# Optimization experiments

Measured on AMD Instinct MI355X. Metric: run time of the kernel, lower is better.

## Reference

```python
import jax, jax.numpy as jnp
import numpy as np

N, L, H, D_HEAD, P = 2, 1024, 8, 64, 1
DIM = H * D_HEAD


def setup_inputs() -> dict:
    key0 = jax.random.key(0)
    ks = jax.random.split(key0, 7)
    query = jax.random.normal(ks[0], (N, L, DIM), dtype=jnp.float32)
    key = jax.random.normal(ks[1], (N, L, DIM), dtype=jnp.float32)
    scale = 1.0 / np.sqrt(DIM)
    Wq = jax.random.normal(ks[2], (DIM, DIM), dtype=jnp.float32) * scale
    Wk = jax.random.normal(ks[3], (DIM, DIM), dtype=jnp.float32) * scale
    Wv = jax.random.normal(ks[4], (DIM, DIM), dtype=jnp.float32) * scale
    position_weight = jax.random.uniform(ks[5], (H, P, D_HEAD), dtype=jnp.float32) * 2 - 1
    position_bias = jax.random.uniform(ks[6], (H, D_HEAD), dtype=jnp.float32) * 2 - 1
    return {"query": query, "key": key, "Wq": Wq, "Wk": Wk, "Wv": Wv,
            "position_weight": position_weight, "position_bias": position_bias}


def _kernel_fn(x):
    # _log_exp_kernel: positive feature map log(1 + exp(x)) (softplus)
    return jax.nn.softplus(x)


def _causal_term(qf, kf, v):
    """Linear-complexity causal attention term.
    qf, kf: (N,H,L,d) feature-mapped query/key; v: (N,H,L,d) values.
    Returns numerator (N,H,L,d) and denominator (N,H,L)."""
    # cumulative key-value outer products: (N,H,L,d,d)
    kv = jnp.cumsum(jnp.einsum('nhkd,nhke->nhkde', kf, v), axis=2)
    num = jnp.einsum('nhqd,nhqde->nhqe', qf, kv)
    den = jnp.einsum('nhqd,nhqd->nhq', qf, jnp.cumsum(kf, axis=2))
    return num, den


def reference(query, key, Wq, Wk, Wv, position_weight, position_bias):
    n, lq, dim = query.shape
    lk = key.shape[1]
    h, p, d = position_weight.shape
    kernel = _kernel_fn
    # projections (torch Linear: x @ W.T), reshape to heads, transpose to (N,H,L,d)
    q = kernel((query @ Wq.T).reshape(n, lq, h, d)).transpose(0, 2, 1, 3)
    k = kernel((key @ Wk.T).reshape(n, lk, h, d)).transpose(0, 2, 1, 3)
    v = ((key @ Wv.T).reshape(n, lk, h, d)).transpose(0, 2, 1, 3)
    # default positions: arange, expanded to (N,L,P)
    qpos = jnp.broadcast_to(jnp.arange(lq, dtype=query.dtype)[None, :, None], (n, lq, p))
    kpos = jnp.broadcast_to(jnp.arange(lk, dtype=key.dtype)[None, :, None], (n, lk, p))
    pq = jnp.einsum('nlp,hpd->nhld', qpos, position_weight) \
         + jax.nn.sigmoid(position_bias)[None, :, None, :] * jnp.pi
    pk = jnp.einsum('nlp,hpd->nhld', kpos, position_weight)
    # three branches: cos, sin, plain (trig identity split of cos(pq - pk) RPE)
    num_c, den_c = _causal_term(q * jnp.cos(pq), k * jnp.cos(pk), v)
    num_s, den_s = _causal_term(q * jnp.sin(pq), k * jnp.sin(pk), v)
    num_p, den_p = _causal_term(q, k, v)
    num = num_c + num_s + num_p
    den = den_c + den_s + den_p
    attention = num / den[..., None]  # scaled=True
    return attention.transpose(0, 2, 1, 3).reshape(n, lq, dim)
```

## Files before the change

### kernel.cpp

```cpp
#include <hip/hip_runtime.h>

#define LSEQ   1024
#define NHEAD  8
#define DH     64
#define DIM    512
#define DF     192
#define LDB    72
#define LDQ    200
#define LDV    72

typedef __attribute__((ext_vector_type(8))) short short8;
typedef __attribute__((ext_vector_type(4))) float floatx4;

__device__ __forceinline__ unsigned short bf16_rne(float x) {
    unsigned int u = __float_as_uint(x);
    u += 0x7FFFu + ((u >> 16) & 1u);
    return (unsigned short)(u >> 16);
}
__device__ __forceinline__ unsigned int pk_bf16(float lo, float hi) {
    unsigned int d;
    asm("v_cvt_pk_bf16_f32 %0, %1, %2" : "=v"(d) : "v"(lo), "v"(hi));
    return d;
}
__device__ __forceinline__ float softplus_fast(float x) {
    return (x > 15.f) ? x : __logf(1.f + __expf(x));
}

__global__ __launch_bounds__(256) void proj_kernel(
    const float* __restrict__ query, const float* __restrict__ key,
    const float* __restrict__ Wq, const float* __restrict__ Wk,
    const float* __restrict__ Wv,
    const float* __restrict__ pw, const float* __restrict__ pb,
    unsigned short* __restrict__ qf, unsigned short* __restrict__ kf,
    unsigned short* __restrict__ vbuf)
{
    const int mt  = blockIdx.x;
    const int ot  = blockIdx.y;
    const int sel = blockIdx.z;
    const int t   = threadIdx.x;

    const float* __restrict__ X = (sel == 0) ? query : key;
    const float* __restrict__ W = (sel == 0) ? Wq : (sel == 1) ? Wk : Wv;

    __shared__ unsigned short As[64 * LDB];
    __shared__ unsigned short Bs[64 * LDB];

    const int m0 = mt * 64, o0 = ot * 64;
    const int lane = t & 63, wave = t >> 6;
    const int quad = lane >> 4, l16 = lane & 15;
    const int wm = wave >> 1, wn = wave & 1;

    const int srow = t >> 2;
    const int sc16 = (t & 3) * 16;

    floatx4 acc[2][2];
    #pragma unroll
    for (int i = 0; i < 2; ++i)
        #pragma unroll
        for (int j = 0; j < 2; ++j) acc[i][j] = (floatx4){0.f, 0.f, 0.f, 0.f};

    float4 ax[4], bx4[4];
    #pragma unroll
    for (int i = 0; i < 4; ++i) {
        ax[i]  = *(const float4*)&X[(size_t)(m0 + srow) * DIM + sc16 + i * 4];
        bx4[i] = *(const float4*)&W[(size_t)(o0 + srow) * DIM + sc16 + i * 4];
    }

    for (int kt = 0; kt < DIM; kt += 64) {
        __syncthreads();
        {
            unsigned int ua[8], ub[8];
            #pragma unroll
            for (int i = 0; i < 4; ++i) {
                ua[2*i]   = pk_bf16(ax[i].x, ax[i].y);
                ua[2*i+1] = pk_bf16(ax[i].z, ax[i].w);
                ub[2*i]   = pk_bf16(bx4[i].x, bx4[i].y);
                ub[2*i+1] = pk_bf16(bx4[i].z, bx4[i].w);
            }
            *(uint4*)&As[srow * LDB + sc16]     = *(uint4*)&ua[0];
            *(uint4*)&As[srow * LDB + sc16 + 8] = *(uint4*)&ua[4];
            *(uint4*)&Bs[srow * LDB + sc16]     = *(uint4*)&ub[0];
            *(uint4*)&Bs[srow * LDB + sc16 + 8] = *(uint4*)&ub[4];
        }
        __syncthreads();

        if (kt + 64 < DIM) {
            #pragma unroll
            for (int i = 0; i < 4; ++i) {
                ax[i]  = *(const float4*)&X[(size_t)(m0 + srow) * DIM + kt + 64 + sc16 + i * 4];
                bx4[i] = *(const float4*)&W[(size_t)(o0 + srow) * DIM + kt + 64 + sc16 + i * 4];
            }
        }

        #pragma unroll
        for (int s = 0; s < 2; ++s) {
            short8 af[2], bf[2];
            #pragma unroll
            for (int mi = 0; mi < 2; ++mi)
                af[mi] = *(const short8*)&As[(wm * 32 + mi * 16 + l16) * LDB + s * 32 + quad * 8];
            #pragma unroll
            for (int ni = 0; ni < 2; ++ni)
                bf[ni] = *(const short8*)&Bs[(wn * 32 + ni * 16 + l16) * LDB + s * 32 + quad * 8];
            #pragma unroll
            for (int ni = 0; ni < 2; ++ni)
                #pragma unroll
                for (int mi = 0; mi < 2; ++mi)
                    acc[mi][ni] = __builtin_amdgcn_mfma_f32_16x16x32_bf16(af[mi], bf[ni], acc[mi][ni], 0, 0, 0);
        }
    }

    const int h = ot;
    const float PI_ = 3.14159265358979323846f;
    const int n_ = m0 >> 10;

    if (sel == 2) {
        __syncthreads();
        #pragma unroll
        for (int mi = 0; mi < 2; ++mi)
            #pragma unroll
            for (int ni = 0; ni < 2; ++ni) {
                const int d = wn * 32 + ni * 16 + l16;
                #pragma unroll
                for (int r = 0; r < 4; ++r) {
                    const int ml = wm * 32 + mi * 16 + quad * 4 + r;
                    As[ml * LDB + d] = bf16_rne(acc[mi][ni][r]);
                }
            }
        __syncthreads();
        const int d = t >> 2, mq = (t & 3) * 16;
        const int l0 = m0 & (LSEQ - 1);
        unsigned short col[16];
        #pragma unroll
        for (int j = 0; j < 16; ++j) col[j] = As[(mq + j) * LDB + d];
        unsigned short* dst = &vbuf[((size_t)(n_ * NHEAD + h) * DH + d) * LSEQ + l0 + mq];
        *(short8*)&dst[0] = *(short8*)&col[0];
        *(short8*)&dst[8] = *(short8*)&col[8];
    } else {
        unsigned short* __restrict__ obuf = (sel == 0) ? qf : kf;
        #pragma unroll
        for (int ni = 0; ni < 2; ++ni) {
            const int d = wn * 32 + ni * 16 + l16;
            const float w = pw[h * DH + d];
            const float bias = (sel == 0) ? PI_ / (1.f + __expf(-pb[h * DH + d])) : 0.f;
            float s1, c1; sincosf(w, &s1, &c1);
            const float c2  = c1*c1 - s1*s1,  s2  = 2.f*c1*s1;
            const float c4  = c2*c2 - s2*s2,  s4  = 2.f*c2*s2;
            const float c8  = c4*c4 - s4*s4,  s8  = 2.f*c4*s4;
            const float c16 = c8*c8 - s8*s8,  s16 = 2.f*c8*s8;
            const int lb = (m0 & (LSEQ - 1)) + wm * 32 + quad * 4;
            float sb, cb; sincosf((float)lb * w + bias, &sb, &cb);
            #pragma unroll
            for (int mi = 0; mi < 2; ++mi) {
                float cc = cb, ss = sb;
                #pragma unroll
                for (int r = 0; r < 4; ++r) {
                    const int l = lb + mi * 16 + r;
                    const float val = softplus_fast(acc[mi][ni][r]);
                    const size_t ob = ((size_t)(n_ * NHEAD + h) * LSEQ + l) * DF + d;
                    obuf[ob]          = bf16_rne(val);
                    obuf[ob + DH]     = bf16_rne(val * cc);
                    obuf[ob + 2*DH]   = bf16_rne(val * ss);
                    const float nc = cc * c1 - ss * s1;
                    ss = ss * c1 + cc * s1; cc = nc;
                }
                const float nb = cb * c16 - sb * s16;
                sb = sb * c16 + cb * s16; cb = nb;
            }
        }
    }
}

__global__ __launch_bounds__(256) void attn_kernel(
    const unsigned short* __restrict__ qf, const unsigned short* __restrict__ kf,
    const unsigned short* __restrict__ vbuf,
    float* __restrict__ outp)
{
    const int b  = blockIdx.x;
    const int nh = (b & 7) * 2 + ((b >> 3) & 1);
    const int p  = (b >> 4) & 15;
    const int z  = b >> 8;
    const int lt = z ? (31 - p) : p;
    const int n  = nh >> 3;
    const int h  = nh & (NHEAD - 1);
    const int t  = threadIdx.x;
    const int lane = t & 63, wave = t >> 6;
    const int quad = lane >> 4, l16 = lane & 15;
    const int wm = wave >> 1, wn = wave & 1;

    __shared__ unsigned short kL[64 * LDQ];
    __shared__ unsigned short vT[64 * LDV];
    __shared__ unsigned short scA[32 * LDV];
    __shared__ float denL[2][32];
    __shared__ float inv32[32];

    const size_t fbase = (size_t)nh * LSEQ;
    const int nkt = (lt >> 1) + 1;
    const int diag_kt = lt >> 1;

    short8 qreg[6];
    {
        const unsigned short* qrow = &qf[(fbase + lt * 32 + wm * 16 + l16) * DF + quad * 8];
        #pragma unroll
        for (int kk = 0; kk < 6; ++kk)
            qreg[kk] = *(const short8*)&qrow[kk * 32];
    }

    int kr[6], kc[6];
    #pragma unroll
    for (int c = 0; c < 6; ++c) {
        const int idx = c * 256 + t;
        kr[c] = idx / 24;
        kc[c] = (idx % 24) * 8;
    }
    const unsigned short* kfb = &kf[fbase * DF];
    const int ve = t >> 2, vk = (t & 3) * 16;
    const unsigned short* vfb = &vbuf[((size_t)nh * DH + ve) * LSEQ + vk];

    short8 kpre[6], vpre[2];
    #pragma unroll
    for (int c = 0; c < 6; ++c)
        kpre[c] = *(const short8*)&kfb[(size_t)kr[c] * DF + kc[c]];
    vpre[0] = *(const short8*)&vfb[0];
    vpre[1] = *(const short8*)&vfb[8];
    #pragma unroll
    for (int c = 0; c < 6; ++c)
        *(short8*)&kL[kr[c] * LDQ + kc[c]] = kpre[c];
    *(short8*)&vT[ve * LDV + vk]     = vpre[0];
    *(short8*)&vT[ve * LDV + vk + 8] = vpre[1];
    __syncthreads();

    floatx4 accN[2];
    accN[0] = (floatx4){0.f, 0.f, 0.f, 0.f};
    accN[1] = (floatx4){0.f, 0.f, 0.f, 0.f};
    float den4[4] = {0.f, 0.f, 0.f, 0.f};

    for (int kt = 0; kt < nkt; ++kt) {
        const bool pf = (kt + 1 < nkt);
        if (pf) {
            const size_t koff = (size_t)(kt + 1) * 64 * DF;
            #pragma unroll
            for (int c = 0; c < 6; ++c)
                kpre[c] = *(const short8*)&kfb[koff + (size_t)kr[c] * DF + kc[c]];
            vpre[0] = *(const short8*)&vfb[(kt + 1) * 64];
            vpre[1] = *(const short8*)&vfb[(kt + 1) * 64 + 8];
        }

        floatx4 accS[2];
        accS[0] = (floatx4){0.f, 0.f, 0.f, 0.f};
        accS[1] = (floatx4){0.f, 0.f, 0.f, 0.f};
        #pragma unroll
        for (int kk = 0; kk < 6; ++kk) {
            #pragma unroll
            for (int ni = 0; ni < 2; ++ni) {
                const short8 bfr = *(const short8*)&kL[(wn * 32 + ni * 16 + l16) * LDQ + kk * 32 + quad * 8];
                accS[ni] = __builtin_amdgcn_mfma_f32_16x16x32_bf16(qreg[kk], bfr, accS[ni], 0, 0, 0);
            }
        }

        const bool diag = (kt == diag_kt);
        #pragma unroll
        for (int ni = 0; ni < 2; ++ni) {
            const int kcolL = wn * 32 + ni * 16 + l16;
            const int kcolG = kt * 64 + kcolL;
            #pragma unroll
            for (int r = 0; r < 4; ++r) {
                const int lrowL = wm * 16 + quad * 4 + r;
                float sval = accS[ni][r];
                if (diag && kcolG > lt * 32 + lrowL) sval = 0.f;
                den4[r] += sval;
                scA[lrowL * LDV + kcolL] = bf16_rne(sval);
            }
        }
        __syncthreads();

        #pragma unroll
        for (int kk = 0; kk < 2; ++kk) {
            const short8 a = *(const short8*)&scA[(wm * 16 + l16) * LDV + kk * 32 + quad * 8];
            #pragma unroll
            for (int ni = 0; ni < 2; ++ni) {
                const short8 bfr = *(const short8*)&vT[(wn * 32 + ni * 16 + l16) * LDV + kk * 32 + quad * 8];
                accN[ni] = __builtin_amdgcn_mfma_f32_16x16x32_bf16(a, bfr, accN[ni], 0, 0, 0);
            }
        }
        __syncthreads();

        if (pf) {
            #pragma unroll
            for (int c = 0; c < 6; ++c)
                *(short8*)&kL[kr[c] * LDQ + kc[c]] = kpre[c];
            *(short8*)&vT[ve * LDV + vk]     = vpre[0];
            *(short8*)&vT[ve * LDV + vk + 8] = vpre[1];
            __syncthreads();
        }
    }

    #pragma unroll
    for (int r = 0; r < 4; ++r) {
        float s = den4[r];
        s += __shfl_xor(s, 1);
        s += __shfl_xor(s, 2);
        s += __shfl_xor(s, 4);
        s += __shfl_xor(s, 8);
        if (l16 == 0) denL[wn][wm * 16 + quad * 4 + r] = s;
    }
    __syncthreads();
    if (t < 32) inv32[t] = 1.f / (denL[0][t] + denL[1][t]);
    __syncthreads();

    #pragma unroll
    for (int ni = 0; ni < 2; ++ni) {
        const int e = wn * 32 + ni * 16 + l16;
        #pragma unroll
        for (int r = 0; r < 4; ++r) {
            const int row = wm * 16 + quad * 4 + r;
            outp[((size_t)n * LSEQ + lt * 32 + row) * DIM + h * DH + e] =
                accN[ni][r] * inv32[row];
        }
    }
}

extern "C" void kernel_launch(void* const* d_in, const int* in_sizes, int n_in,
                              void* d_out, int out_size, void* d_ws, size_t ws_size,
                              hipStream_t stream) {
    const float* query = (const float*)d_in[0];
    const float* key   = (const float*)d_in[1];
    const float* Wq    = (const float*)d_in[2];
    const float* Wk    = (const float*)d_in[3];
    const float* Wv    = (const float*)d_in[4];
    const float* pw    = (const float*)d_in[5];
    const float* pb    = (const float*)d_in[6];

    unsigned short* U = (unsigned short*)d_ws;
    unsigned short* qf   = U;
    unsigned short* kf   = U + 3145728;
    unsigned short* vbuf = U + 6291456;

    proj_kernel<<<dim3(32, 8, 3), 256, 0, stream>>>(
        query, key, Wq, Wk, Wv, pw, pb, qf, kf, vbuf);
    attn_kernel<<<dim3(512, 1, 1), 256, 0, stream>>>(
        qf, kf, vbuf, (float*)d_out);
}
```

Baseline: 105.4 us.

## Halve query tile to 16 rows and double attention grid

The attention kernel now gives each block a 16-row query tile instead of 32 and launches 1024 blocks instead of 512. Each wave handles one 16-column slice of the key tile rather than a 2x2 wave grid, and the launch bounds ask for 4 blocks per CU. MFMA sections are wrapped in s_setprio to favour matrix issue. This raises parallelism and occupancy on the causal triangular workload, but every K/V tile is now loaded from global memory twice as often in total, and the work per barrier is smaller.

```diff
diff --git a/kernel.cpp b/kernel.cpp
--- a/kernel.cpp
+++ b/kernel.cpp
@@ -170,36 +170,35 @@
     }
 }
 
-__global__ __launch_bounds__(256) void attn_kernel(
+__global__ __launch_bounds__(256, 4) void attn_kernel(
     const unsigned short* __restrict__ qf, const unsigned short* __restrict__ kf,
     const unsigned short* __restrict__ vbuf,
     float* __restrict__ outp)
 {
     const int b  = blockIdx.x;
     const int nh = (b & 7) * 2 + ((b >> 3) & 1);
-    const int p  = (b >> 4) & 15;
-    const int z  = b >> 8;
-    const int lt = z ? (31 - p) : p;
+    const int p  = (b >> 4) & 31;
+    const int z  = b >> 9;
+    const int lt = z ? (63 - p) : p;
     const int n  = nh >> 3;
     const int h  = nh & (NHEAD - 1);
     const int t  = threadIdx.x;
-    const int lane = t & 63, wave = t >> 6;
+    const int lane = t & 63, w = t >> 6;
     const int quad = lane >> 4, l16 = lane & 15;
-    const int wm = wave >> 1, wn = wave & 1;
 
     __shared__ unsigned short kL[64 * LDQ];
     __shared__ unsigned short vT[64 * LDV];
-    __shared__ unsigned short scA[32 * LDV];
-    __shared__ float denL[2][32];
-    __shared__ float inv32[32];
+    __shared__ unsigned short scA[16 * LDV];
+    __shared__ float denW[4][16];
+    __shared__ float inv16[16];
 
     const size_t fbase = (size_t)nh * LSEQ;
-    const int nkt = (lt >> 1) + 1;
-    const int diag_kt = lt >> 1;
+    const int nkt = (lt >> 2) + 1;
+    const int diag_kt = lt >> 2;
 
     short8 qreg[6];
     {
-        const unsigned short* qrow = &qf[(fbase + lt * 32 + wm * 16 + l16) * DF + quad * 8];
+        const unsigned short* qrow = &qf[(fbase + lt * 16 + l16) * DF + quad * 8];
         #pragma unroll
         for (int kk = 0; kk < 6; ++kk)
             qreg[kk] = *(const short8*)&qrow[kk * 32];
@@ -229,9 +228,7 @@
     *(short8*)&vT[ve * LDV + vk + 8] = vpre[1];
     __syncthreads();
 
-    floatx4 accN[2];
-    accN[0] = (floatx4){0.f, 0.f, 0.f, 0.f};
-    accN[1] = (floatx4){0.f, 0.f, 0.f, 0.f};
+    floatx4 accN = (floatx4){0.f, 0.f, 0.f, 0.f};
     float den4[4] = {0.f, 0.f, 0.f, 0.f};
 
     for (int kt = 0; kt < nkt; ++kt) {
@@ -245,43 +242,36 @@
             vpre[1] = *(const short8*)&vfb[(kt + 1) * 64 + 8];
         }
 
-        floatx4 accS[2];
-        accS[0] = (floatx4){0.f, 0.f, 0.f, 0.f};
-        accS[1] = (floatx4){0.f, 0.f, 0.f, 0.f};
+        floatx4 accS = (floatx4){0.f, 0.f, 0.f, 0.f};
+        __builtin_amdgcn_s_setprio(1);
         #pragma unroll
         for (int kk = 0; kk < 6; ++kk) {
-            #pragma unroll
-            for (int ni = 0; ni < 2; ++ni) {
-                const short8 bfr = *(const short8*)&kL[(wn * 32 + ni * 16 + l16) * LDQ + kk * 32 + quad * 8];
-                accS[ni] = __builtin_amdgcn_mfma_f32_16x16x32_bf16(qreg[kk], bfr, accS[ni], 0, 0, 0);
-            }
-        }
+            const short8 bfr = *(const short8*)&kL[(w * 16 + l16) * LDQ + kk * 32 + quad * 8];
+            accS = __builtin_amdgcn_mfma_f32_16x16x32_bf16(qreg[kk], bfr, accS, 0, 0, 0);
+        }
+        __builtin_amdgcn_s_setprio(0);
 
         const bool diag = (kt == diag_kt);
-        #pragma unroll
-        for (int ni = 0; ni < 2; ++ni) {
-            const int kcolL = wn * 32 + ni * 16 + l16;
-            const int kcolG = kt * 64 + kcolL;
-            #pragma unroll
-            for (int r = 0; r < 4; ++r) {
-                const int lrowL = wm * 16 + quad * 4 + r;
-                float sval = accS[ni][r];
-                if (diag && kcolG > lt * 32 + lrowL) sval = 0.f;
-                den4[r] += sval;
-                scA[lrowL * LDV + kcolL] = bf16_rne(sval);
-            }
-        }
-        __syncthreads();
-
+        const int kcolL = w * 16 + l16;
+        const int kcolG = kt * 64 + kcolL;
+        #pragma unroll
+        for (int r = 0; r < 4; ++r) {
+            const int row = quad * 4 + r;
+            float sval = accS[r];
+            if (diag && kcolG > lt * 16 + row) sval = 0.f;
+            den4[r] += sval;
+            scA[row * LDV + kcolL] = bf16_rne(sval);
+        }
+        __syncthreads();
+
+        __builtin_amdgcn_s_setprio(1);
         #pragma unroll
         for (int kk = 0; kk < 2; ++kk) {
-            const short8 a = *(const short8*)&scA[(wm * 16 + l16) * LDV + kk * 32 + quad * 8];
-            #pragma unroll
-            for (int ni = 0; ni < 2; ++ni) {
-                const short8 bfr = *(const short8*)&vT[(wn * 32 + ni * 16 + l16) * LDV + kk * 32 + quad * 8];
-                accN[ni] = __builtin_amdgcn_mfma_f32_16x16x32_bf16(a, bfr, accN[ni], 0, 0, 0);
-            }
-        }
+            const short8 a   = *(const short8*)&scA[l16 * LDV + kk * 32 + quad * 8];
+            const short8 bfr = *(const short8*)&vT[(w * 16 + l16) * LDV + kk * 32 + quad * 8];
+            accN = __builtin_amdgcn_mfma_f32_16x16x32_bf16(a, bfr, accN, 0, 0, 0);
+        }
+        __builtin_amdgcn_s_setprio(0);
         __syncthreads();
 
         if (pf) {
@@ -301,20 +291,19 @@
         s += __shfl_xor(s, 2);
         s += __shfl_xor(s, 4);
         s += __shfl_xor(s, 8);
-        if (l16 == 0) denL[wn][wm * 16 + quad * 4 + r] = s;
+        if (l16 == 0) denW[w][quad * 4 + r] = s;
     }
     __syncthreads();
-    if (t < 32) inv32[t] = 1.f / (denL[0][t] + denL[1][t]);
+    if (t < 16) inv16[t] = 1.f / (denW[0][t] + denW[1][t] + denW[2][t] + denW[3][t]);
     __syncthreads();
 
-    #pragma unroll
-    for (int ni = 0; ni < 2; ++ni) {
-        const int e = wn * 32 + ni * 16 + l16;
+    {
+        const int e = w * 16 + l16;
         #pragma unroll
         for (int r = 0; r < 4; ++r) {
-            const int row = wm * 16 + quad * 4 + r;
-            outp[((size_t)n * LSEQ + lt * 32 + row) * DIM + h * DH + e] =
-                accN[ni][r] * inv32[row];
+            const int row = quad * 4 + r;
+            outp[((size_t)n * LSEQ + lt * 16 + row) * DIM + h * DH + e] =
+                accN[r] * inv16[row];
         }
     }
 }
@@ -337,6 +326,6 @@
 
     proj_kernel<<<dim3(32, 8, 3), 256, 0, stream>>>(
         query, key, Wq, Wk, Wv, pw, pb, qf, kf, vbuf);
-    attn_kernel<<<dim3(512, 1, 1), 256, 0, stream>>>(
+    attn_kernel<<<dim3(1024, 1, 1), 256, 0, stream>>>(
         qf, kf, vbuf, (float*)d_out);
 }
```

New measurement: 108.8 us. 3.2% more time.

## Double-buffer K/V shared tiles and prefetch two tiles ahead

Applied to the files above, without the earlier changes.

Splits the K and V shared-memory tiles into two ping-pong buffers. While one buffer is consumed, the register-staged next tile is written into the other, and the global loads for the tile after that are issued. This drops one __syncthreads per iteration and gives the global loads more compute to hide behind. In exchange, the K/V shared-memory footprint doubles, which may lower occupancy.

```diff
diff --git a/kernel.cpp b/kernel.cpp
--- a/kernel.cpp
+++ b/kernel.cpp
@@ -187,8 +187,8 @@
     const int quad = lane >> 4, l16 = lane & 15;
     const int wm = wave >> 1, wn = wave & 1;
 
-    __shared__ unsigned short kL[64 * LDQ];
-    __shared__ unsigned short vT[64 * LDV];
+    __shared__ unsigned short kL[2][64 * LDQ];
+    __shared__ unsigned short vT[2][64 * LDV];
     __shared__ unsigned short scA[32 * LDV];
     __shared__ float denL[2][32];
     __shared__ float inv32[32];
@@ -224,9 +224,17 @@
     vpre[1] = *(const short8*)&vfb[8];
     #pragma unroll
     for (int c = 0; c < 6; ++c)
-        *(short8*)&kL[kr[c] * LDQ + kc[c]] = kpre[c];
-    *(short8*)&vT[ve * LDV + vk]     = vpre[0];
-    *(short8*)&vT[ve * LDV + vk + 8] = vpre[1];
+        *(short8*)&kL[0][kr[c] * LDQ + kc[c]] = kpre[c];
+    *(short8*)&vT[0][ve * LDV + vk]     = vpre[0];
+    *(short8*)&vT[0][ve * LDV + vk + 8] = vpre[1];
+    if (nkt > 1) {
+        const size_t koff = (size_t)64 * DF;
+        #pragma unroll
+        for (int c = 0; c < 6; ++c)
+            kpre[c] = *(const short8*)&kfb[koff + (size_t)kr[c] * DF + kc[c]];
+        vpre[0] = *(const short8*)&vfb[64];
+        vpre[1] = *(const short8*)&vfb[64 + 8];
+    }
     __syncthreads();
 
     floatx4 accN[2];
@@ -235,15 +243,10 @@
     float den4[4] = {0.f, 0.f, 0.f, 0.f};
 
     for (int kt = 0; kt < nkt; ++kt) {
+        const int cur = kt & 1;
+        const unsigned short* kLc = &kL[cur][0];
+        const unsigned short* vTc = &vT[cur][0];
         const bool pf = (kt + 1 < nkt);
-        if (pf) {
-            const size_t koff = (size_t)(kt + 1) * 64 * DF;
-            #pragma unroll
-            for (int c = 0; c < 6; ++c)
-                kpre[c] = *(const short8*)&kfb[koff + (size_t)kr[c] * DF + kc[c]];
-            vpre[0] = *(const short8*)&vfb[(kt + 1) * 64];
-            vpre[1] = *(const short8*)&vfb[(kt + 1) * 64 + 8];
-        }
 
         floatx4 accS[2];
         accS[0] = (floatx4){0.f, 0.f, 0.f, 0.f};
@@ -252,7 +255,7 @@
         for (int kk = 0; kk < 6; ++kk) {
             #pragma unroll
             for (int ni = 0; ni < 2; ++ni) {
-                const short8 bfr = *(const short8*)&kL[(wn * 32 + ni * 16 + l16) * LDQ + kk * 32 + quad * 8];
+                const short8 bfr = *(const short8*)&kLc[(wn * 32 + ni * 16 + l16) * LDQ + kk * 32 + quad * 8];
                 accS[ni] = __builtin_amdgcn_mfma_f32_16x16x32_bf16(qreg[kk], bfr, accS[ni], 0, 0, 0);
             }
         }
@@ -273,25 +276,34 @@
         }
         __syncthreads();
 
+        if (pf) {
+            unsigned short* kLn = &kL[cur ^ 1][0];
+            unsigned short* vTn = &vT[cur ^ 1][0];
+            #pragma unroll
+            for (int c = 0; c < 6; ++c)
+                *(short8*)&kLn[kr[c] * LDQ + kc[c]] = kpre[c];
+            *(short8*)&vTn[ve * LDV + vk]     = vpre[0];
+            *(short8*)&vTn[ve * LDV + vk + 8] = vpre[1];
+            if (kt + 2 < nkt) {
+                const size_t koff = (size_t)(kt + 2) * 64 * DF;
+                #pragma unroll
+                for (int c = 0; c < 6; ++c)
+                    kpre[c] = *(const short8*)&kfb[koff + (size_t)kr[c] * DF + kc[c]];
+                vpre[0] = *(const short8*)&vfb[(kt + 2) * 64];
+                vpre[1] = *(const short8*)&vfb[(kt + 2) * 64 + 8];
+            }
+        }
+
         #pragma unroll
         for (int kk = 0; kk < 2; ++kk) {
             const short8 a = *(const short8*)&scA[(wm * 16 + l16) * LDV + kk * 32 + quad * 8];
             #pragma unroll
             for (int ni = 0; ni < 2; ++ni) {
-                const short8 bfr = *(const short8*)&vT[(wn * 32 + ni * 16 + l16) * LDV + kk * 32 + quad * 8];
+                const short8 bfr = *(const short8*)&vTc[(wn * 32 + ni * 16 + l16) * LDV + kk * 32 + quad * 8];
                 accN[ni] = __builtin_amdgcn_mfma_f32_16x16x32_bf16(a, bfr, accN[ni], 0, 0, 0);
             }
         }
         __syncthreads();
-
-        if (pf) {
-            #pragma unroll
-            for (int c = 0; c < 6; ++c)
-                *(short8*)&kL[kr[c] * LDQ + kc[c]] = kpre[c];
-            *(short8*)&vT[ve * LDV + vk]     = vpre[0];
-            *(short8*)&vT[ve * LDV + vk + 8] = vpre[1];
-            __syncthreads();
-        }
     }
 
     #pragma unroll
```

Result: slower. 110.8 us (+5.1%).

## Split PV matmul along key dim per wave to drop a barrier

Applied to the files above, without the earlier changes.

Each wave now multiplies only the score columns it produced (its own 32-key half) against all 64 value columns, instead of reading the full score tile after a block barrier. This removes one __syncthreads per key tile, since a wave only consumes scA entries it wrote itself. In exchange, each wave keeps four accumulators instead of two, and the two key-half partial results are reduced through a new shared-memory buffer at the end, with only half the waves writing output.

```diff
diff --git a/kernel.cpp b/kernel.cpp
--- a/kernel.cpp
+++ b/kernel.cpp
@@ -190,6 +190,7 @@
     __shared__ unsigned short kL[64 * LDQ];
     __shared__ unsigned short vT[64 * LDV];
     __shared__ unsigned short scA[32 * LDV];
+    __shared__ float nsum[2][16][64];
     __shared__ float denL[2][32];
     __shared__ float inv32[32];
 
@@ -229,9 +230,9 @@
     *(short8*)&vT[ve * LDV + vk + 8] = vpre[1];
     __syncthreads();
 
-    floatx4 accN[2];
-    accN[0] = (floatx4){0.f, 0.f, 0.f, 0.f};
-    accN[1] = (floatx4){0.f, 0.f, 0.f, 0.f};
+    floatx4 accN[4];
+    #pragma unroll
+    for (int ei = 0; ei < 4; ++ei) accN[ei] = (floatx4){0.f, 0.f, 0.f, 0.f};
     float den4[4] = {0.f, 0.f, 0.f, 0.f};
 
     for (int kt = 0; kt < nkt; ++kt) {
@@ -271,15 +272,13 @@
                 scA[lrowL * LDV + kcolL] = bf16_rne(sval);
             }
         }
-        __syncthreads();
-
-        #pragma unroll
-        for (int kk = 0; kk < 2; ++kk) {
-            const short8 a = *(const short8*)&scA[(wm * 16 + l16) * LDV + kk * 32 + quad * 8];
-            #pragma unroll
-            for (int ni = 0; ni < 2; ++ni) {
-                const short8 bfr = *(const short8*)&vT[(wn * 32 + ni * 16 + l16) * LDV + kk * 32 + quad * 8];
-                accN[ni] = __builtin_amdgcn_mfma_f32_16x16x32_bf16(a, bfr, accN[ni], 0, 0, 0);
+
+        {
+            const short8 a = *(const short8*)&scA[(wm * 16 + l16) * LDV + wn * 32 + quad * 8];
+            #pragma unroll
+            for (int ei = 0; ei < 4; ++ei) {
+                const short8 bfr = *(const short8*)&vT[(ei * 16 + l16) * LDV + wn * 32 + quad * 8];
+                accN[ei] = __builtin_amdgcn_mfma_f32_16x16x32_bf16(a, bfr, accN[ei], 0, 0, 0);
             }
         }
         __syncthreads();
@@ -303,19 +302,27 @@
         s += __shfl_xor(s, 8);
         if (l16 == 0) denL[wn][wm * 16 + quad * 4 + r] = s;
     }
+    if (wn == 1) {
+        #pragma unroll
+        for (int ei = 0; ei < 4; ++ei)
+            #pragma unroll
+            for (int r = 0; r < 4; ++r)
+                nsum[wm][quad * 4 + r][ei * 16 + l16] = accN[ei][r];
+    }
     __syncthreads();
     if (t < 32) inv32[t] = 1.f / (denL[0][t] + denL[1][t]);
     __syncthreads();
 
-    #pragma unroll
-    for (int ni = 0; ni < 2; ++ni) {
-        const int e = wn * 32 + ni * 16 + l16;
-        #pragma unroll
-        for (int r = 0; r < 4; ++r) {
-            const int row = wm * 16 + quad * 4 + r;
-            outp[((size_t)n * LSEQ + lt * 32 + row) * DIM + h * DH + e] =
-                accN[ni][r] * inv32[row];
-        }
+    if (wn == 0) {
+        #pragma unroll
+        for (int ei = 0; ei < 4; ++ei)
+            #pragma unroll
+            for (int r = 0; r < 4; ++r) {
+                const int row = wm * 16 + quad * 4 + r;
+                const float v = (accN[ei][r] + nsum[wm][quad * 4 + r][ei * 16 + l16])
+                                * inv32[row];
+                outp[((size_t)n * LSEQ + lt * 32 + row) * DIM + h * DH + ei * 16 + l16] = v;
+            }
     }
 }
 
```

Measured after the change: 107.6 us. 2.1% more time.
